# Optimization experiments

Hardware: AMD Instinct MI355X
Metric: run time of the kernel (lower is better)

## Reference

```python
import jax, jax.numpy as jnp
import numpy as np

NEG_INF = -jnp.inf
EPS = 1e-12  # F.normalize eps


def _build_spans(text_mask_row, max_span_length):
    # text_mask_row: concrete bool array [S]. Returns static numpy span index arrays.
    pos = np.nonzero(np.asarray(text_mask_row))[0]
    n = pos.size
    starts, ends, lens = [], [], []
    for i in range(n):
        for j in range(i, min(i + max_span_length, n)):
            starts.append(pos[i]); ends.append(pos[j]); lens.append(j - i + 1)
    return (np.asarray(starts, np.int32), np.asarray(ends, np.int32), np.asarray(lens, np.int32))


def setup_inputs() -> dict:
    key = jax.random.key(0)
    ks = jax.random.split(key, 8)
    B, S, H, T = 16, 1024, 768, 64
    L, LE = 4, 32
    Din = 3 * H + LE
    return {
        "hidden_states": jax.random.normal(ks[0], (B, S, H), jnp.float32),
        "topic_hidden": jax.random.normal(ks[1], (B, T, H), jnp.float32),
        "topic_mask": jnp.ones((B, T), jnp.bool_),
        "text_mask": jnp.ones((B, S), jnp.bool_),
        "len_emb": jax.random.normal(ks[2], (L + 1, LE), jnp.float32) * 0.02,
        "W1": jax.random.normal(ks[3], (Din, H), jnp.float32) / np.sqrt(Din),
        "b1": jnp.zeros((H,), jnp.float32),
        "W2": jax.random.normal(ks[4], (H, H), jnp.float32) / np.sqrt(H),
        "b2": jnp.zeros((H,), jnp.float32),
    }


def _l2norm(x):
    n = jnp.sqrt(jnp.sum(x * x, axis=-1, keepdims=True))
    return x / jnp.maximum(n, EPS)


def reference(hidden_states, topic_hidden, topic_mask, text_mask, len_emb, W1, b1, W2, b2):
    B, S, H = hidden_states.shape
    max_span_length = len_emb.shape[0] - 1
    # Masks are identical across the batch (all ones here): build spans once.
    starts_np, ends_np, lens_np = _build_spans(text_mask[0], max_span_length)
    starts = jnp.asarray(starts_np); ends = jnp.asarray(ends_np); lens = jnp.asarray(lens_np)
    N = starts.shape[0]

    start_v = hidden_states[:, starts]          # [B,N,H] gather span starts
    end_v = hidden_states[:, ends]              # [B,N,H] gather span ends
    csum = jnp.concatenate([jnp.zeros((B, 1, H), hidden_states.dtype),
                            jnp.cumsum(hidden_states, axis=1)], axis=1)  # [B,S+1,H]
    mean_v = (csum[:, ends + 1] - csum[:, starts]) / lens[None, :, None].astype(hidden_states.dtype)
    len_v = jnp.broadcast_to(len_emb[lens][None], (B, N, len_emb.shape[1]))

    feat = jnp.concatenate([start_v, end_v, mean_v, len_v], axis=-1)  # [B,N,3H+LE]
    span_vec = jax.nn.gelu(feat @ W1 + b1, approximate=False) @ W2 + b2  # [B,N,H]
    span_vec = _l2norm(span_vec)
    topic_vec = _l2norm(topic_hidden)                                    # [B,T,H]

    sim = jnp.einsum('bth,bnh->btn', topic_vec, span_vec)                # [B,T,N]
    sim = jnp.where(topic_mask[:, :, None], sim, NEG_INF)
    span_scores = jnp.max(sim, axis=1)                                   # [B,N]

    tok = jnp.arange(S)
    cover = (tok[None, :] >= starts[:, None]) & (tok[None, :] <= ends[:, None])  # [N,S]
    token_scores = jnp.max(jnp.where(cover[None], span_scores[:, :, None], NEG_INF), axis=1)  # [B,S]
    token_scores = jnp.where(text_mask, token_scores, NEG_INF)
    return token_scores
```

## Files before the change

### kernel.cpp

```cpp
#include <hip/hip_runtime.h>
#include <hip/hip_bf16.h>
#include <math.h>

typedef __bf16 bf16s;
typedef __attribute__((ext_vector_type(8))) __bf16 bf16x8;
typedef __attribute__((ext_vector_type(4))) __bf16 bf16x4;
typedef __attribute__((ext_vector_type(4))) float f32x4;

#define B_   16
#define S_   1024
#define H_   768
#define T_   64
#define L_   4
#define LE_  32
#define NPAD 4096
#define BS   (B_*S_)
#define BNR  (B_*NPAD)
#define N3   (3*H_)

static __device__ __forceinline__ void gload_lds16(const void* g, void* l) {
  __builtin_amdgcn_global_load_lds(
      (const __attribute__((address_space(1))) void*)g,
      (__attribute__((address_space(3))) void*)l, 16, 0, 0);
}

__global__ __launch_bounds__(1024) void k_build_spans(
    const int* __restrict__ text_mask,
    int* __restrict__ R, int* __restrict__ pos, int* __restrict__ spoff,
    int* __restrict__ starts, int* __restrict__ ends, int* __restrict__ lens,
    int* __restrict__ meta)
{
  __shared__ int buf[S_];
  int t = threadIdx.x;
  int m = text_mask[t] ? 1 : 0;
  buf[t] = m;
  __syncthreads();
  for (int off = 1; off < S_; off <<= 1) {
    int v = buf[t];
    if (t >= off) v += buf[t - off];
    __syncthreads();
    buf[t] = v;
    __syncthreads();
  }
  int incl = buf[t];
  R[t] = incl;
  if (m) pos[incl - 1] = t;
  int n = buf[S_ - 1];
  __syncthreads();
  int cnt = (t < n) ? min(L_, n - t) : 0;
  buf[t] = cnt;
  __syncthreads();
  for (int off = 1; off < S_; off <<= 1) {
    int v = buf[t];
    if (t >= off) v += buf[t - off];
    __syncthreads();
    buf[t] = v;
    __syncthreads();
  }
  int inc2 = buf[t];
  int base = inc2 - cnt;
  spoff[t] = base;
  if (t == 0) { meta[0] = buf[S_ - 1]; meta[1] = n; }
  __syncthreads();
  if (t < n) {
    int p0 = pos[t];
    for (int k = 0; k < cnt; k++) {
      starts[base + k] = p0;
      ends[base + k]   = pos[t + k];
      lens[base + k]   = k + 1;
    }
  }
}

__global__ __launch_bounds__(256) void k_prep(
    const float* __restrict__ hid, bf16s* __restrict__ hidb,
    const float* __restrict__ W1, bf16s* __restrict__ wbt,
    const float* __restrict__ W2, bf16s* __restrict__ w2t, bf16s* __restrict__ w2c,
    const float* __restrict__ lemb, float* __restrict__ LT,
    const float* __restrict__ TH, const float* __restrict__ b2,
    bf16s* __restrict__ TN, float* __restrict__ cvec)
{
  __shared__ float tile[64][65];
  __shared__ float red[256];
  int bid = blockIdx.x;
  int t = threadIdx.x;
  if (bid < 12288) {
    int i = bid * 256 + t;
    f32x4 v = ((const f32x4*)hid)[i];
    bf16x4 o;
    o[0] = (__bf16)v[0]; o[1] = (__bf16)v[1]; o[2] = (__bf16)v[2]; o[3] = (__bf16)v[3];
    ((bf16x4*)hidb)[i] = o;
  } else if (bid < 12864) {
    int local = bid - 12288;
    int c = local / 144, rem = local % 144;
    const float* in = (c < 3) ? (W1 + (size_t)c * H_ * H_) : W2;
    bf16s* out = (c < 3) ? (wbt + (size_t)c * H_ * H_) : w2t;
    int r0 = (rem / 12) * 64, c0 = (rem % 12) * 64;
    int tr = t >> 4, tc = (t & 15) * 4;
#pragma unroll
    for (int i = 0; i < 4; i++) {
      int row = tr + i * 16;
      f32x4 v = *(const f32x4*)(in + (long)(r0 + row) * H_ + c0 + tc);
      tile[row][tc+0] = v[0]; tile[row][tc+1] = v[1];
      tile[row][tc+2] = v[2]; tile[row][tc+3] = v[3];
    }
    __syncthreads();
#pragma unroll
    for (int i = 0; i < 4; i++) {
      int cc = tr + i * 16;
      bf16x4 o;
      o[0] = (__bf16)tile[tc+0][cc]; o[1] = (__bf16)tile[tc+1][cc];
      o[2] = (__bf16)tile[tc+2][cc]; o[3] = (__bf16)tile[tc+3][cc];
      *(bf16x4*)(out + (long)(c0 + cc) * H_ + r0 + tc) = o;
    }
  } else if (bid < 13440) {
    int i = (bid - 12864) * 256 + t;
    f32x4 v = ((const f32x4*)W2)[i];
    bf16x4 o;
    o[0] = (__bf16)v[0]; o[1] = (__bf16)v[1]; o[2] = (__bf16)v[2]; o[3] = (__bf16)v[3];
    ((bf16x4*)w2c)[i] = o;
  } else if (bid < 13455) {
    int idx = (bid - 13440) * 256 + t;
    if (idx < (L_ + 1) * H_) {
      int l = idx / H_, h = idx % H_;
      float acc = 0.f;
#pragma unroll
      for (int e = 0; e < LE_; e++) acc += lemb[l * LE_ + e] * W1[(long)(N3 + e) * H_ + h];
      LT[idx] = acc;
    }
  } else {
    int r = bid - 13455;
    const float* row = TH + (long)r * H_;
    float v0 = row[t], v1 = row[t + 256], v2 = row[t + 512];
    red[t] = v0 * v0 + v1 * v1 + v2 * v2;
    __syncthreads();
    for (int off = 128; off; off >>= 1) {
      if (t < off) red[t] += red[t + off];
      __syncthreads();
    }
    float rn = 1.0f / fmaxf(sqrtf(red[0]), 1e-12f);
    bf16s* o = TN + (long)r * H_;
    o[t] = (__bf16)(v0 * rn); o[t + 256] = (__bf16)(v1 * rn); o[t + 512] = (__bf16)(v2 * rn);
    __syncthreads();
    red[t] = v0 * b2[t] + v1 * b2[t + 256] + v2 * b2[t + 512];
    __syncthreads();
    for (int off = 128; off; off >>= 1) {
      if (t < off) red[t] += red[t + off];
      __syncthreads();
    }
    if (t == 0) cvec[r] = red[0] * rn;
  }
}

#define BKT 64
#define STG_A(kt_, h_) do { \
    const bf16s* s_ = gA + (long)(h_) * 128 * K + (long)(kt_) * BKT; \
    char* d_ = sA + ((kt_) & 1) * 32768 + (h_) * 16384 + wid * 1024; \
    gload_lds16(s_, d_); \
    gload_lds16(s_ + 64L * K, d_ + 8192); \
  } while (0)
#define STG_B(ct_, kt_, h_) do { \
    const bf16s* s_ = gB + (long)(ct_) * 256 * K + (long)(h_) * 128 * K + (long)(kt_) * BKT; \
    char* d_ = sB + ((kt_) & 1) * 32768 + (h_) * 16384 + wid * 1024; \
    gload_lds16(s_, d_); \
    gload_lds16(s_ + 64L * K, d_ + 8192); \
  } while (0)
#define MFMA_Q(AF_, FR0_, FC_) do { \
    _Pragma("unroll") \
    for (int f_ = 0; f_ < 4; ++f_) { \
      acc[FR0_+f_][FC_] = __builtin_amdgcn_mfma_f32_16x16x32_bf16(bfv[FC_][0], AF_[f_][0], acc[FR0_+f_][FC_], 0, 0, 0); \
      acc[FR0_+f_][FC_] = __builtin_amdgcn_mfma_f32_16x16x32_bf16(bfv[FC_][1], AF_[f_][1], acc[FR0_+f_][FC_], 0, 0, 0); \
    } } while (0)
#define PH_PRE()  __builtin_amdgcn_s_barrier(); \
                  asm volatile("s_waitcnt lgkmcnt(0)" ::: "memory"); \
                  __builtin_amdgcn_s_setprio(1)
#define PH_POST() __builtin_amdgcn_s_setprio(0); \
                  __builtin_amdgcn_s_barrier()

#define CHAIN_CORE(EPILOG_) \
  const char* aP0 = sA + wr * 16384; \
  const char* aP1 = aP0 + 32768; \
  const char* bP0 = sB + (wc >> 1) * 16384 + (wc & 1) * 8192; \
  const char* bP1 = bP0 + 32768; \
  int lrow = (l & 15) * 128; \
  int ls0 = (((l >> 4) ^ (l & 7)) * 16); \
  f32x4 acc[8][4]; \
  _Pragma("unroll") \
  for (int i_ = 0; i_ < 8; i_++) \
    _Pragma("unroll") \
    for (int j_ = 0; j_ < 4; j_++) acc[i_][j_] = (f32x4){0.f, 0.f, 0.f, 0.f}; \
  STG_B(0, 0, 0); STG_B(0, 0, 1); STG_A(0, 0); STG_A(0, 1); \
  STG_B(0, 1, 0); STG_B(0, 1, 1); STG_A(1, 0); \
  asm volatile("s_waitcnt vmcnt(6)" ::: "memory"); \
  __builtin_amdgcn_s_barrier(); \
  for (int s = 0; s < 3; ++s) { \
    for (int it = 0; it < 6; ++it) { \
      int kt0 = 2 * it; \
      bool nl = !(s == 2 && it == 5); \
      int ctn = (it == 5) ? s + 1 : s; \
      int kn0 = (it == 5) ? 0 : kt0 + 2; \
      int kn1 = (it == 5) ? 1 : kt0 + 3; \
      bf16x8 af0[4][2], af1[4][2], bfv[4][2]; \
       \
      _Pragma("unroll") \
      for (int f = 0; f < 4; ++f) { \
        af0[f][0] = *(const bf16x8*)(aP0 + f * 2048 + lrow + ls0); \
        af0[f][1] = *(const bf16x8*)(aP0 + f * 2048 + lrow + (ls0 ^ 64)); \
      } \
      _Pragma("unroll") \
      for (int c = 0; c < 4; ++c) { \
        bfv[c][0] = *(const bf16x8*)(bP0 + c * 2048 + lrow + ls0); \
        bfv[c][1] = *(const bf16x8*)(bP0 + c * 2048 + lrow + (ls0 ^ 64)); \
      } \
      STG_A(kt0 + 1, 1); \
      PH_PRE(); \
      MFMA_Q(af0, 0, 0); MFMA_Q(af0, 0, 1); \
      PH_POST(); \
       \
      if (nl) STG_B(ctn, kn0, 0); \
      PH_PRE(); \
      MFMA_Q(af0, 0, 2); MFMA_Q(af0, 0, 3); \
      PH_POST(); \
       \
      _Pragma("unroll") \
      for (int f = 0; f < 4; ++f) { \
        af1[f][0] = *(const bf16x8*)(aP0 + (f + 4) * 2048 + lrow + ls0); \
        af1[f][1] = *(const bf16x8*)(aP0 + (f + 4) * 2048 + lrow + (ls0 ^ 64)); \
      } \
      if (nl) STG_B(ctn, kn0, 1); \
      PH_PRE(); \
      MFMA_Q(af1, 4, 0); MFMA_Q(af1, 4, 1); \
      PH_POST(); \
       \
      if (nl) { STG_A(kn0, 0); asm volatile("s_waitcnt vmcnt(6)" ::: "memory"); } \
      else    { asm volatile("s_waitcnt vmcnt(0)" ::: "memory"); } \
      PH_PRE(); \
      MFMA_Q(af1, 4, 2); MFMA_Q(af1, 4, 3); \
      PH_POST(); \
       \
      _Pragma("unroll") \
      for (int f = 0; f < 4; ++f) { \
        af0[f][0] = *(const bf16x8*)(aP1 + f * 2048 + lrow + ls0); \
        af0[f][1] = *(const bf16x8*)(aP1 + f * 2048 + lrow + (ls0 ^ 64)); \
      } \
      _Pragma("unroll") \
      for (int c = 0; c < 4; ++c) { \
        bfv[c][0] = *(const bf16x8*)(bP1 + c * 2048 + lrow + ls0); \
        bfv[c][1] = *(const bf16x8*)(bP1 + c * 2048 + lrow + (ls0 ^ 64)); \
      } \
      if (nl) STG_A(kn0, 1); \
      PH_PRE(); \
      MFMA_Q(af0, 0, 0); MFMA_Q(af0, 0, 1); \
      PH_POST(); \
       \
      if (nl) STG_B(ctn, kn1, 0); \
      PH_PRE(); \
      MFMA_Q(af0, 0, 2); MFMA_Q(af0, 0, 3); \
      PH_POST(); \
       \
      _Pragma("unroll") \
      for (int f = 0; f < 4; ++f) { \
        af1[f][0] = *(const bf16x8*)(aP1 + (f + 4) * 2048 + lrow + ls0); \
        af1[f][1] = *(const bf16x8*)(aP1 + (f + 4) * 2048 + lrow + (ls0 ^ 64)); \
      } \
      if (nl) STG_B(ctn, kn1, 1); \
      PH_PRE(); \
      MFMA_Q(af1, 4, 0); MFMA_Q(af1, 4, 1); \
      PH_POST(); \
       \
      if (nl) { STG_A(kn1, 0); asm volatile("s_waitcnt vmcnt(6)" ::: "memory"); } \
      else    { asm volatile("s_waitcnt vmcnt(0)" ::: "memory"); } \
      PH_PRE(); \
      MFMA_Q(af1, 4, 2); MFMA_Q(af1, 4, 3); \
      PH_POST(); \
    } \
    EPILOG_(s); \
  }

__global__ __launch_bounds__(512, 1) void k_gemm1u(
    const bf16s* __restrict__ Ah, const bf16s* __restrict__ Bth, bf16s* __restrict__ Ch,
    const bf16s* __restrict__ Au, const bf16s* __restrict__ Btu, bf16s* __restrict__ Cu)
{
  __shared__ __align__(16) char sA[65536];
  __shared__ __align__(16) char sB[65536];
  __shared__ __align__(16) char sC[16384];
  const int K = H_;
  int bid = blockIdx.x;
  const bf16s *A, *Bt;
  bf16s* C;
  long a0, b0base;
  int NN;
  if (bid < 192) {
    int nid = (bid & 7) * 24 + (bid >> 3);
    A = Ah; Bt = Bth; C = Ch; NN = N3;
    a0 = (long)(nid / 3) * 256;
    b0base = (long)(nid % 3) * 768;
  } else {
    A = Au; Bt = Btu; C = Cu; NN = H_;
    a0 = (long)(bid - 192) * 256;
    b0base = 0;
  }
  int tid = threadIdx.x;
  int wid = tid >> 6, l = tid & 63;
  int wr = wid >> 2, wc = wid & 3;
  int srow = tid >> 3;
  int sslot = (tid & 7) ^ (srow & 7);
  const bf16s* gA = A + (a0 + srow) * (long)K + sslot * 8;
  const bf16s* gB = Bt + (b0base + srow) * (long)K + sslot * 8;

#define EPI_C(s_) do { \
    long cb = b0base + (s_) * 256; \
    _Pragma("unroll") \
    for (int e = 0; e < 8; ++e) { \
      if (wr == (e >> 2)) { \
        int f0 = (e & 3) * 2; \
        _Pragma("unroll") \
        for (int ff = 0; ff < 2; ++ff) { \
          int fr = f0 + ff; \
          int row_l = ff * 16 + (l & 15); \
          _Pragma("unroll") \
          for (int fc = 0; fc < 4; ++fc) { \
            int col2 = (wc * 64 + fc * 16 + (l >> 4) * 4) * 2; \
            bf16x4 o; \
            _Pragma("unroll") \
            for (int r = 0; r < 4; ++r) o[r] = (__bf16)acc[fr][fc][r]; \
            *(bf16x4*)(sC + ((row_l * 512 + col2) ^ ((row_l & 7) << 4))) = o; \
          } \
        } \
      } \
      __syncthreads(); \
      _Pragma("unroll") \
      for (int pp = 0; pp < 2; ++pp) { \
        int off = pp * 8192 + tid * 16; \
        int row_l = off >> 9; \
        bf16x8 v = *(const bf16x8*)(sC + (off ^ ((row_l & 7) << 4))); \
        *(bf16x8*)(C + (a0 + e * 32 + row_l) * (long)NN + cb + ((off & 511) >> 1)) = v; \
      } \
      __syncthreads(); \
    } \
    _Pragma("unroll") \
    for (int i_ = 0; i_ < 8; i_++) \
      _Pragma("unroll") \
      for (int j_ = 0; j_ < 4; j_++) acc[i_][j_] = (f32x4){0.f, 0.f, 0.f, 0.f}; \
  } while (0)

  CHAIN_CORE(EPI_C)
#undef EPI_C
}

__global__ __launch_bounds__(512, 1) void k_gemmnorm(
    const bf16s* __restrict__ Ax, const bf16s* __restrict__ Btw,
    const float* __restrict__ bias, float* __restrict__ ssbuf)
{
  __shared__ __align__(16) char sA[65536];
  __shared__ __align__(16) char sB[65536];
  const int K = H_;
  int bid = blockIdx.x;
  int nid = (bid & 7) * 32 + (bid >> 3);
  long a0 = (long)nid * 256;
  long b0base = 0;
  int tid = threadIdx.x;
  int wid = tid >> 6, l = tid & 63;
  int wr = wid >> 2, wc = wid & 3;
  int srow = tid >> 3;
  int sslot = (tid & 7) ^ (srow & 7);
  const bf16s* gA = Ax + (a0 + srow) * (long)K + sslot * 8;
  const bf16s* gB = Btw + (b0base + srow) * (long)K + sslot * 8;
  float ssp[8] = {0.f, 0.f, 0.f, 0.f, 0.f, 0.f, 0.f, 0.f};

#define EPI_N(s_) do { \
    f32x4 bb[4]; \
    _Pragma("unroll") \
    for (int fc = 0; fc < 4; ++fc) \
      bb[fc] = *(const f32x4*)(bias + (s_) * 256 + wc * 64 + fc * 16 + (l >> 4) * 4); \
    _Pragma("unroll") \
    for (int fr = 0; fr < 8; ++fr) { \
      float p = 0.f; \
      _Pragma("unroll") \
      for (int fc = 0; fc < 4; ++fc) { \
        _Pragma("unroll") \
        for (int r = 0; r < 4; ++r) { \
          float y = acc[fr][fc][r] + bb[fc][r]; \
          p += y * y; \
        } \
        acc[fr][fc] = (f32x4){0.f, 0.f, 0.f, 0.f}; \
      } \
      ssp[fr] += p; \
    } \
  } while (0)

  CHAIN_CORE(EPI_N)
#undef EPI_N

  float* sred = (float*)sA;
#pragma unroll
  for (int fr = 0; fr < 8; ++fr) {
    float p = ssp[fr];
    p += __shfl_xor(p, 16);
    p += __shfl_xor(p, 32);
    if (l < 16) sred[wc * 256 + wr * 128 + fr * 16 + l] = p;
  }
  __syncthreads();
  if (tid < 256) {
    ssbuf[a0 + tid] = sred[tid] + sred[256 + tid] + sred[512 + tid] + sred[768 + tid];
  }
}

#undef CHAIN_CORE
#undef STG_A
#undef STG_B
#undef MFMA_Q
#undef PH_PRE
#undef PH_POST

__global__ __launch_bounds__(256) void k_z1(
    const bf16s* __restrict__ P,
    const float* __restrict__ LT, const float* __restrict__ b1,
    const int* __restrict__ starts, const int* __restrict__ ends,
    const int* __restrict__ lens, const int* __restrict__ meta,
    bf16s* __restrict__ X)
{
  int idx = blockIdx.x * 256 + threadIdx.x;
  int h8 = idx % 96; int rest = idx / 96;
  int nid = rest % NPAD; int b = rest / NPAD;
  int h = h8 * 8;
  int N = meta[0];
  long orow = (long)(b * NPAD + nid) * H_ + h;
  if (nid >= N) {
    bf16x8 z;
#pragma unroll
    for (int j = 0; j < 8; j++) z[j] = (__bf16)0.f;
    *(bf16x8*)(X + orow) = z;
    return;
  }
  int sa = starts[nid], se = ends[nid], ln = lens[nid];
  float il = 1.0f / (float)ln;
  bf16x8 vs = *(const bf16x8*)(P + (long)(b * S_ + sa) * N3 + h);
  bf16x8 ve = *(const bf16x8*)(P + (long)(b * S_ + se) * N3 + H_ + h);
  float mv[8] = {0.f, 0.f, 0.f, 0.f, 0.f, 0.f, 0.f, 0.f};
  for (int i = sa; i <= se; i++) {
    bf16x8 vc = *(const bf16x8*)(P + (long)(b * S_ + i) * N3 + 2 * H_ + h);
#pragma unroll
    for (int j = 0; j < 8; j++) mv[j] += (float)vc[j];
  }
  f32x4 lt0 = *(const f32x4*)(LT + (long)ln * H_ + h);
  f32x4 lt1 = *(const f32x4*)(LT + (long)ln * H_ + h + 4);
  f32x4 bb0 = *(const f32x4*)(b1 + h);
  f32x4 bb1 = *(const f32x4*)(b1 + h + 4);
  bf16x8 o;
#pragma unroll
  for (int j = 0; j < 8; j++) {
    float ltv = (j < 4) ? lt0[j] : lt1[j - 4];
    float bbv = (j < 4) ? bb0[j] : bb1[j - 4];
    float x = (float)vs[j] + (float)ve[j] + mv[j] * il + ltv + bbv;
    float g = 0.5f * x * (1.0f + erff(x * 0.70710678118654752f));
    o[j] = (__bf16)g;
  }
  *(bf16x8*)(X + orow) = o;
}

__global__ __launch_bounds__(256) void k_simx(
    const bf16s* __restrict__ X, const bf16s* __restrict__ U,
    const float* __restrict__ cvec, const float* __restrict__ ssbuf,
    const int* __restrict__ tmask, float* __restrict__ scores)
{
  int b = blockIdx.y;
  int wid = threadIdx.x >> 6, l = threadIdx.x & 63;
  int st = blockIdx.x * 4 + wid;
  int span = st * 16 + (l & 15);
  const bf16s* xrow = X + (long)(b * NPAD + span) * H_ + (l >> 4) * 8;
  const bf16s* ubase = U + (long)b * T_ * H_ + (l >> 4) * 8;
  f32x4 acc[4];
#pragma unroll
  for (int tt = 0; tt < 4; tt++) acc[tt] = (f32x4){0.f, 0.f, 0.f, 0.f};
  for (int kk = 0; kk < H_ / 32; kk++) {
    bf16x8 av = *(const bf16x8*)(xrow + kk * 32);
#pragma unroll
    for (int tt = 0; tt < 4; tt++) {
      bf16x8 bv = *(const bf16x8*)(ubase + (long)(tt * 16 + (l & 15)) * H_ + kk * 32);
      acc[tt] = __builtin_amdgcn_mfma_f32_16x16x32_bf16(av, bv, acc[tt], 0, 0, 0);
    }
  }
  const int* tm = tmask + b * T_;
  bool msk[4];
  float cv[4];
#pragma unroll
  for (int tt = 0; tt < 4; tt++) {
    int tcol = tt * 16 + (l & 15);
    msk[tt] = tm[tcol] != 0;
    cv[tt] = cvec[b * T_ + tcol];
  }
  float best[4];
#pragma unroll
  for (int r = 0; r < 4; r++) {
    float v = -INFINITY;
#pragma unroll
    for (int tt = 0; tt < 4; tt++) if (msk[tt]) v = fmaxf(v, acc[tt][r] + cv[tt]);
    best[r] = v;
  }
#pragma unroll
  for (int off = 8; off; off >>= 1)
#pragma unroll
    for (int r = 0; r < 4; r++) best[r] = fmaxf(best[r], __shfl_xor(best[r], off));
  if ((l & 15) == 0) {
    int srow = st * 16 + (l >> 4) * 4;
#pragma unroll
    for (int r = 0; r < 4; r++) {
      float ss = ssbuf[b * NPAD + srow + r];
      scores[b * NPAD + srow + r] = best[r] / fmaxf(sqrtf(ss), 1e-12f);
    }
  }
}

__global__ __launch_bounds__(256) void k_token(
    const int* __restrict__ text_mask,
    const int* __restrict__ R, const int* __restrict__ spoff,
    const int* __restrict__ meta, const float* __restrict__ scores,
    float* __restrict__ out)
{
  int idx = blockIdx.x * 256 + threadIdx.x;
  int s = idx % S_, b = idx / S_;
  if (!text_mask[b * S_ + s]) { out[idx] = -INFINITY; return; }
  int n = meta[1];
  int r1 = R[s];
  int le = r1 - 1;
  int ge = text_mask[s] ? (r1 - 1) : r1;
  float best = -INFINITY;
  if (le >= 0 && ge < n) {
    int i0 = max(0, ge - (L_ - 1));
    for (int i = i0; i <= le; i++) {
      int jmax = min(i + L_ - 1, n - 1);
      int off = spoff[i];
      for (int j = max(i, ge); j <= jmax; j++)
        best = fmaxf(best, scores[b * NPAD + off + (j - i)]);
    }
  }
  out[idx] = best;
}

__global__ __launch_bounds__(256) void k_sentinel(float* __restrict__ out) {
  int i = blockIdx.x * 256 + threadIdx.x;
  if (i < BS) out[i] = 12345.0f;
}

extern "C" void kernel_launch(void* const* d_in, const int* in_sizes, int n_in,
                              void* d_out, int out_size, void* d_ws, size_t ws_size,
                              hipStream_t stream) {
  const float* hid = (const float*)d_in[0];
  const float* th  = (const float*)d_in[1];
  const int* tmask = (const int*)d_in[2];
  const int* xmask = (const int*)d_in[3];
  const float* lemb = (const float*)d_in[4];
  const float* W1   = (const float*)d_in[5];
  const float* b1   = (const float*)d_in[6];
  const float* W2   = (const float*)d_in[7];
  const float* b2   = (const float*)d_in[8];
  float* out = (float*)d_out;

  char* w = (char*)d_ws;
  auto alloc = [&](size_t bytes) {
    char* p = w; w += (bytes + 255) & ~(size_t)255; return p;
  };
  bf16s* wbt   = (bf16s*)alloc((size_t)N3 * H_ * 2);
  bf16s* w2t   = (bf16s*)alloc((size_t)H_ * H_ * 2);
  bf16s* w2c   = (bf16s*)alloc((size_t)H_ * H_ * 2);
  float* LT    = (float*)alloc((size_t)(L_ + 1) * H_ * 4);
  bf16s* topn  = (bf16s*)alloc((size_t)B_ * T_ * H_ * 2);
  bf16s* U     = (bf16s*)alloc((size_t)B_ * T_ * H_ * 2);
  float* cvec  = (float*)alloc((size_t)B_ * T_ * 4);
  float* ssbuf = (float*)alloc((size_t)BNR * 4);
  float* scores= (float*)alloc((size_t)B_ * NPAD * 4);
  int* R       = (int*)alloc(S_ * 4);
  int* pos     = (int*)alloc(S_ * 4);
  int* spoff   = (int*)alloc(S_ * 4);
  int* starts  = (int*)alloc(NPAD * 4);
  int* ends    = (int*)alloc(NPAD * 4);
  int* lens    = (int*)alloc(NPAD * 4);
  int* meta    = (int*)alloc(2 * 4);
  char* regionA = alloc((size_t)BS * H_ * 2 + (size_t)BS * N3 * 2);
  bf16s* hidb  = (bf16s*)regionA;
  bf16s* P     = (bf16s*)(regionA + (size_t)BS * H_ * 2);
  bf16s* X     = (bf16s*)alloc((size_t)BNR * H_ * 2);

  size_t required = (size_t)(w - (char*)d_ws);
  if (required > ws_size) {
    k_sentinel<<<(BS + 255) / 256, 256, 0, stream>>>(out);
    return;
  }

  k_build_spans<<<1, 1024, 0, stream>>>(xmask, R, pos, spoff, starts, ends, lens, meta);
  k_prep<<<14479, 256, 0, stream>>>(hid, hidb, W1, wbt, W2, w2t, w2c,
                                    lemb, LT, th, b2, topn, cvec);

  k_gemm1u<<<196, 512, 0, stream>>>(hidb, wbt, P, topn, w2c, U);

  k_z1<<<(BNR * 96) / 256, 256, 0, stream>>>(P, LT, b1, starts, ends, lens, meta, X);

  k_gemmnorm<<<256, 512, 0, stream>>>(X, w2t, b2, ssbuf);

  k_simx<<<dim3(NPAD / 64, B_), 256, 0, stream>>>(X, U, cvec, ssbuf, tmask, scores);
  k_token<<<(B_ * S_) / 256, 256, 0, stream>>>(xmask, R, spoff, meta, scores, out);
  (void)in_sizes; (void)n_in; (void)out_size;
}
```

Baseline: 322.1 us.

## Split first GEMM into per-tile blocks and fuse span-feature build per start token

```diff
diff --git a/kernel.cpp b/kernel.cpp
--- a/kernel.cpp
+++ b/kernel.cpp
@@ -153,14 +153,14 @@
 }
 
 #define BKT 64
-#define STG_A(kt_, h_) do { \
+#define STG1_A(kt_, h_) do { \
     const bf16s* s_ = gA + (long)(h_) * 128 * K + (long)(kt_) * BKT; \
     char* d_ = sA + ((kt_) & 1) * 32768 + (h_) * 16384 + wid * 1024; \
     gload_lds16(s_, d_); \
     gload_lds16(s_ + 64L * K, d_ + 8192); \
   } while (0)
-#define STG_B(ct_, kt_, h_) do { \
-    const bf16s* s_ = gB + (long)(ct_) * 256 * K + (long)(h_) * 128 * K + (long)(kt_) * BKT; \
+#define STG1_B(kt_, h_) do { \
+    const bf16s* s_ = gB + (long)(h_) * 128 * K + (long)(kt_) * BKT; \
     char* d_ = sB + ((kt_) & 1) * 32768 + (h_) * 16384 + wid * 1024; \
     gload_lds16(s_, d_); \
     gload_lds16(s_ + 64L * K, d_ + 8192); \
@@ -176,6 +176,176 @@
                   __builtin_amdgcn_s_setprio(1)
 #define PH_POST() __builtin_amdgcn_s_setprio(0); \
                   __builtin_amdgcn_s_barrier()
+
+__global__ __launch_bounds__(512, 2) void k_gemm8p(
+    const bf16s* __restrict__ Ah, const bf16s* __restrict__ Bth, bf16s* __restrict__ Ch,
+    const bf16s* __restrict__ Au, const bf16s* __restrict__ Btu, bf16s* __restrict__ Cu)
+{
+  __shared__ __align__(16) char sA[65536];
+  __shared__ __align__(16) char sB[65536];
+  const int K = H_;
+
+  int nwg = gridDim.x, bid = blockIdx.x;
+  int q = nwg >> 3, rr = nwg & 7;
+  int xcd = bid & 7, ix = bid >> 3;
+  int nid = (xcd < rr ? xcd * (q + 1) : rr * (q + 1) + (xcd - rr) * q) + ix;
+
+  const bf16s *A, *Bt;
+  bf16s* C;
+  long a0, b0;
+  int NN;
+  if (nid < 576) {
+    A = Ah; Bt = Bth; C = Ch; NN = N3;
+    a0 = (long)(nid / 9) * 256;
+    b0 = (long)(nid % 9) * 256;
+  } else {
+    int u = nid - 576;
+    A = Au; Bt = Btu; C = Cu; NN = H_;
+    a0 = (long)(u / 3) * 256;
+    b0 = (long)(u % 3) * 256;
+  }
+
+  int tid = threadIdx.x;
+  int wid = tid >> 6, l = tid & 63;
+  int wr = wid >> 2, wc = wid & 3;
+
+  int srow = tid >> 3;
+  int sslot = (tid & 7) ^ (srow & 7);
+  const bf16s* gA = A + (a0 + srow) * (long)K + sslot * 8;
+  const bf16s* gB = Bt + (b0 + srow) * (long)K + sslot * 8;
+
+  const char* aP0 = sA + wr * 16384;
+  const char* aP1 = aP0 + 32768;
+  const char* bP0 = sB + (wc >> 1) * 16384 + (wc & 1) * 8192;
+  const char* bP1 = bP0 + 32768;
+  int lrow = (l & 15) * 128;
+  int ls0 = (((l >> 4) ^ (l & 7)) * 16);
+
+  f32x4 acc[8][4];
+#pragma unroll
+  for (int i = 0; i < 8; i++)
+#pragma unroll
+    for (int j = 0; j < 4; j++) acc[i][j] = (f32x4){0.f, 0.f, 0.f, 0.f};
+
+  int NT = K / BKT;
+  int NITER = NT / 2;
+
+  STG1_B(0, 0); STG1_B(0, 1); STG1_A(0, 0); STG1_A(0, 1);
+  STG1_B(1, 0); STG1_B(1, 1); STG1_A(1, 0);
+  asm volatile("s_waitcnt vmcnt(6)" ::: "memory");
+  __builtin_amdgcn_s_barrier();
+
+  for (int it = 0; it < NITER; ++it) {
+    int t0 = 2 * it, t1 = t0 + 1;
+    bool nl = (it != NITER - 1);
+    bf16x8 af0[4][2], af1[4][2], bfv[4][2];
+
+#pragma unroll
+    for (int f = 0; f < 4; ++f) {
+      af0[f][0] = *(const bf16x8*)(aP0 + f * 2048 + lrow + ls0);
+      af0[f][1] = *(const bf16x8*)(aP0 + f * 2048 + lrow + (ls0 ^ 64));
+    }
+#pragma unroll
+    for (int c = 0; c < 4; ++c) {
+      bfv[c][0] = *(const bf16x8*)(bP0 + c * 2048 + lrow + ls0);
+      bfv[c][1] = *(const bf16x8*)(bP0 + c * 2048 + lrow + (ls0 ^ 64));
+    }
+    STG1_A(t1, 1);
+    PH_PRE();
+    MFMA_Q(af0, 0, 0); MFMA_Q(af0, 0, 1);
+    PH_POST();
+
+    if (nl) STG1_B(t0 + 2, 0);
+    PH_PRE();
+    MFMA_Q(af0, 0, 2); MFMA_Q(af0, 0, 3);
+    PH_POST();
+
+#pragma unroll
+    for (int f = 0; f < 4; ++f) {
+      af1[f][0] = *(const bf16x8*)(aP0 + (f + 4) * 2048 + lrow + ls0);
+      af1[f][1] = *(const bf16x8*)(aP0 + (f + 4) * 2048 + lrow + (ls0 ^ 64));
+    }
+    if (nl) STG1_B(t0 + 2, 1);
+    PH_PRE();
+    MFMA_Q(af1, 4, 0); MFMA_Q(af1, 4, 1);
+    PH_POST();
+
+    if (nl) { STG1_A(t0 + 2, 0); asm volatile("s_waitcnt vmcnt(6)" ::: "memory"); }
+    else    { asm volatile("s_waitcnt vmcnt(0)" ::: "memory"); }
+    PH_PRE();
+    MFMA_Q(af1, 4, 2); MFMA_Q(af1, 4, 3);
+    PH_POST();
+
+#pragma unroll
+    for (int f = 0; f < 4; ++f) {
+      af0[f][0] = *(const bf16x8*)(aP1 + f * 2048 + lrow + ls0);
+      af0[f][1] = *(const bf16x8*)(aP1 + f * 2048 + lrow + (ls0 ^ 64));
+    }
+#pragma unroll
+    for (int c = 0; c < 4; ++c) {
+      bfv[c][0] = *(const bf16x8*)(bP1 + c * 2048 + lrow + ls0);
+      bfv[c][1] = *(const bf16x8*)(bP1 + c * 2048 + lrow + (ls0 ^ 64));
+    }
+    if (nl) STG1_A(t0 + 2, 1);
+    PH_PRE();
+    MFMA_Q(af0, 0, 0); MFMA_Q(af0, 0, 1);
+    PH_POST();
+
+    if (nl) STG1_B(t1 + 2, 0);
+    PH_PRE();
+    MFMA_Q(af0, 0, 2); MFMA_Q(af0, 0, 3);
+    PH_POST();
+
+#pragma unroll
+    for (int f = 0; f < 4; ++f) {
+      af1[f][0] = *(const bf16x8*)(aP1 + (f + 4) * 2048 + lrow + ls0);
+      af1[f][1] = *(const bf16x8*)(aP1 + (f + 4) * 2048 + lrow + (ls0 ^ 64));
+    }
+    if (nl) STG1_B(t1 + 2, 1);
+    PH_PRE();
+    MFMA_Q(af1, 4, 0); MFMA_Q(af1, 4, 1);
+    PH_POST();
+
+    if (nl) { STG1_A(t1 + 2, 0); asm volatile("s_waitcnt vmcnt(6)" ::: "memory"); }
+    else    { asm volatile("s_waitcnt vmcnt(0)" ::: "memory"); }
+    PH_PRE();
+    MFMA_Q(af1, 4, 2); MFMA_Q(af1, 4, 3);
+    PH_POST();
+  }
+
+#pragma unroll
+  for (int fc = 0; fc < 4; fc++) {
+    long n0 = b0 + wc * 64 + fc * 16 + (l >> 4) * 4;
+#pragma unroll
+    for (int fr = 0; fr < 8; fr++) {
+      long mrow = a0 + wr * 128 + fr * 16 + (l & 15);
+      bf16x4 o;
+#pragma unroll
+      for (int r = 0; r < 4; r++) o[r] = (__bf16)acc[fr][fc][r];
+      *(bf16x4*)(C + mrow * (long)NN + n0) = o;
+    }
+  }
+}
+
+#define STG_A(kt_, h_) do { \
+    const bf16s* s_ = gA + (long)(h_) * 128 * K + (long)(kt_) * BKT; \
+    char* d_ = sA + ((kt_) & 1) * 32768 + (h_) * 16384 + wid * 1024; \
+    gload_lds16(s_, d_); \
+    gload_lds16(s_ + 64L * K, d_ + 8192); \
+  } while (0)
+#define STG_B(ct_, kt_, h_) do { \
+    const bf16s* s_ = gB + (long)(ct_) * 256 * K + (long)(h_) * 128 * K + (long)(kt_) * BKT; \
+    char* d_ = sB + ((kt_) & 1) * 32768 + (h_) * 16384 + wid * 1024; \
+    gload_lds16(s_, d_); \
+    gload_lds16(s_ + 8192); \
+  } while (0)
+#undef STG_B
+#define STG_B(ct_, kt_, h_) do { \
+    const bf16s* s_ = gB + (long)(ct_) * 256 * K + (long)(h_) * 128 * K + (long)(kt_) * BKT; \
+    char* d_ = sB + ((kt_) & 1) * 32768 + (h_) * 16384 + wid * 1024; \
+    gload_lds16(s_, d_); \
+    gload_lds16(s_ + 64L * K, d_ + 8192); \
+  } while (0)
 
 #define CHAIN_CORE(EPILOG_) \
   const char* aP0 = sA + wr * 16384; \
@@ -201,7 +371,6 @@
       int kn0 = (it == 5) ? 0 : kt0 + 2; \
       int kn1 = (it == 5) ? 1 : kt0 + 3; \
       bf16x8 af0[4][2], af1[4][2], bfv[4][2]; \
-       \
       _Pragma("unroll") \
       for (int f = 0; f < 4; ++f) { \
         af0[f][0] = *(const bf16x8*)(aP0 + f * 2048 + lrow + ls0); \
@@ -216,12 +385,10 @@
       PH_PRE(); \
       MFMA_Q(af0, 0, 0); MFMA_Q(af0, 0, 1); \
       PH_POST(); \
-       \
       if (nl) STG_B(ctn, kn0, 0); \
       PH_PRE(); \
       MFMA_Q(af0, 0, 2); MFMA_Q(af0, 0, 3); \
       PH_POST(); \
-       \
       _Pragma("unroll") \
       for (int f = 0; f < 4; ++f) { \
         af1[f][0] = *(const bf16x8*)(aP0 + (f + 4) * 2048 + lrow + ls0); \
@@ -231,13 +398,11 @@
       PH_PRE(); \
       MFMA_Q(af1, 4, 0); MFMA_Q(af1, 4, 1); \
       PH_POST(); \
-       \
       if (nl) { STG_A(kn0, 0); asm volatile("s_waitcnt vmcnt(6)" ::: "memory"); } \
       else    { asm volatile("s_waitcnt vmcnt(0)" ::: "memory"); } \
       PH_PRE(); \
       MFMA_Q(af1, 4, 2); MFMA_Q(af1, 4, 3); \
       PH_POST(); \
-       \
       _Pragma("unroll") \
       for (int f = 0; f < 4; ++f) { \
         af0[f][0] = *(const bf16x8*)(aP1 + f * 2048 + lrow + ls0); \
@@ -252,12 +417,10 @@
       PH_PRE(); \
       MFMA_Q(af0, 0, 0); MFMA_Q(af0, 0, 1); \
       PH_POST(); \
-       \
       if (nl) STG_B(ctn, kn1, 0); \
       PH_PRE(); \
       MFMA_Q(af0, 0, 2); MFMA_Q(af0, 0, 3); \
       PH_POST(); \
-       \
       _Pragma("unroll") \
       for (int f = 0; f < 4; ++f) { \
         af1[f][0] = *(const bf16x8*)(aP1 + (f + 4) * 2048 + lrow + ls0); \
@@ -267,7 +430,6 @@
       PH_PRE(); \
       MFMA_Q(af1, 4, 0); MFMA_Q(af1, 4, 1); \
       PH_POST(); \
-       \
       if (nl) { STG_A(kn1, 0); asm volatile("s_waitcnt vmcnt(6)" ::: "memory"); } \
       else    { asm volatile("s_waitcnt vmcnt(0)" ::: "memory"); } \
       PH_PRE(); \
@@ -276,77 +438,6 @@
     } \
     EPILOG_(s); \
   }
-
-__global__ __launch_bounds__(512, 1) void k_gemm1u(
-    const bf16s* __restrict__ Ah, const bf16s* __restrict__ Bth, bf16s* __restrict__ Ch,
-    const bf16s* __restrict__ Au, const bf16s* __restrict__ Btu, bf16s* __restrict__ Cu)
-{
-  __shared__ __align__(16) char sA[65536];
-  __shared__ __align__(16) char sB[65536];
-  __shared__ __align__(16) char sC[16384];
-  const int K = H_;
-  int bid = blockIdx.x;
-  const bf16s *A, *Bt;
-  bf16s* C;
-  long a0, b0base;
-  int NN;
-  if (bid < 192) {
-    int nid = (bid & 7) * 24 + (bid >> 3);
-    A = Ah; Bt = Bth; C = Ch; NN = N3;
-    a0 = (long)(nid / 3) * 256;
-    b0base = (long)(nid % 3) * 768;
-  } else {
-    A = Au; Bt = Btu; C = Cu; NN = H_;
-    a0 = (long)(bid - 192) * 256;
-    b0base = 0;
-  }
-  int tid = threadIdx.x;
-  int wid = tid >> 6, l = tid & 63;
-  int wr = wid >> 2, wc = wid & 3;
-  int srow = tid >> 3;
-  int sslot = (tid & 7) ^ (srow & 7);
-  const bf16s* gA = A + (a0 + srow) * (long)K + sslot * 8;
-  const bf16s* gB = Bt + (b0base + srow) * (long)K + sslot * 8;
-
-#define EPI_C(s_) do { \
-    long cb = b0base + (s_) * 256; \
-    _Pragma("unroll") \
-    for (int e = 0; e < 8; ++e) { \
-      if (wr == (e >> 2)) { \
-        int f0 = (e & 3) * 2; \
-        _Pragma("unroll") \
-        for (int ff = 0; ff < 2; ++ff) { \
-          int fr = f0 + ff; \
-          int row_l = ff * 16 + (l & 15); \
-          _Pragma("unroll") \
-          for (int fc = 0; fc < 4; ++fc) { \
-            int col2 = (wc * 64 + fc * 16 + (l >> 4) * 4) * 2; \
-            bf16x4 o; \
-            _Pragma("unroll") \
-            for (int r = 0; r < 4; ++r) o[r] = (__bf16)acc[fr][fc][r]; \
-            *(bf16x4*)(sC + ((row_l * 512 + col2) ^ ((row_l & 7) << 4))) = o; \
-          } \
-        } \
-      } \
-      __syncthreads(); \
-      _Pragma("unroll") \
-      for (int pp = 0; pp < 2; ++pp) { \
-        int off = pp * 8192 + tid * 16; \
-        int row_l = off >> 9; \
-        bf16x8 v = *(const bf16x8*)(sC + (off ^ ((row_l & 7) << 4))); \
-        *(bf16x8*)(C + (a0 + e * 32 + row_l) * (long)NN + cb + ((off & 511) >> 1)) = v; \
-      } \
-      __syncthreads(); \
-    } \
-    _Pragma("unroll") \
-    for (int i_ = 0; i_ < 8; i_++) \
-      _Pragma("unroll") \
-      for (int j_ = 0; j_ < 4; j_++) acc[i_][j_] = (f32x4){0.f, 0.f, 0.f, 0.f}; \
-  } while (0)
-
-  CHAIN_CORE(EPI_C)
-#undef EPI_C
-}
 
 __global__ __launch_bounds__(512, 1) void k_gemmnorm(
     const bf16s* __restrict__ Ax, const bf16s* __restrict__ Btw,
@@ -409,54 +500,66 @@
 #undef CHAIN_CORE
 #undef STG_A
 #undef STG_B
+#undef STG1_A
+#undef STG1_B
 #undef MFMA_Q
 #undef PH_PRE
 #undef PH_POST
 
-__global__ __launch_bounds__(256) void k_z1(
+__global__ __launch_bounds__(192) void k_z1(
     const bf16s* __restrict__ P,
     const float* __restrict__ LT, const float* __restrict__ b1,
-    const int* __restrict__ starts, const int* __restrict__ ends,
-    const int* __restrict__ lens, const int* __restrict__ meta,
-    bf16s* __restrict__ X)
+    const int* __restrict__ pos, const int* __restrict__ spoff,
+    const int* __restrict__ meta, bf16s* __restrict__ X)
 {
-  int idx = blockIdx.x * 256 + threadIdx.x;
-  int h8 = idx % 96; int rest = idx / 96;
-  int nid = rest % NPAD; int b = rest / NPAD;
-  int h = h8 * 8;
-  int N = meta[0];
-  long orow = (long)(b * NPAD + nid) * H_ + h;
-  if (nid >= N) {
-    bf16x8 z;
-#pragma unroll
-    for (int j = 0; j < 8; j++) z[j] = (__bf16)0.f;
-    *(bf16x8*)(X + orow) = z;
-    return;
-  }
-  int sa = starts[nid], se = ends[nid], ln = lens[nid];
-  float il = 1.0f / (float)ln;
-  bf16x8 vs = *(const bf16x8*)(P + (long)(b * S_ + sa) * N3 + h);
-  bf16x8 ve = *(const bf16x8*)(P + (long)(b * S_ + se) * N3 + H_ + h);
-  float mv[8] = {0.f, 0.f, 0.f, 0.f, 0.f, 0.f, 0.f, 0.f};
-  for (int i = sa; i <= se; i++) {
-    bf16x8 vc = *(const bf16x8*)(P + (long)(b * S_ + i) * N3 + 2 * H_ + h);
-#pragma unroll
-    for (int j = 0; j < 8; j++) mv[j] += (float)vc[j];
-  }
-  f32x4 lt0 = *(const f32x4*)(LT + (long)ln * H_ + h);
-  f32x4 lt1 = *(const f32x4*)(LT + (long)ln * H_ + h + 4);
-  f32x4 bb0 = *(const f32x4*)(b1 + h);
-  f32x4 bb1 = *(const f32x4*)(b1 + h + 4);
-  bf16x8 o;
-#pragma unroll
-  for (int j = 0; j < 8; j++) {
-    float ltv = (j < 4) ? lt0[j] : lt1[j - 4];
-    float bbv = (j < 4) ? bb0[j] : bb1[j - 4];
-    float x = (float)vs[j] + (float)ve[j] + mv[j] * il + ltv + bbv;
-    float g = 0.5f * x * (1.0f + erff(x * 0.70710678118654752f));
-    o[j] = (__bf16)g;
-  }
-  *(bf16x8*)(X + orow) = o;
+  int bid = blockIdx.x;
+  int t = threadIdx.x;
+  int h = t * 4;
+  if (bid < BS) {
+    int b = bid >> 10, i = bid & (S_ - 1);
+    int n = meta[1];
+    if (i >= n) return;
+    int cnt = min(L_, n - i);
+    int sa = pos[i];
+    int base = spoff[i];
+    const bf16s* Pb = P + (long)b * S_ * N3;
+    bf16x4 vs = *(const bf16x4*)(Pb + (long)sa * N3 + h);
+    f32x4 bb = *(const f32x4*)(b1 + h);
+    float run[4] = {0.f, 0.f, 0.f, 0.f};
+    int r = sa;
+    for (int k = 0; k < cnt; ++k) {
+      int se = pos[i + k];
+      for (; r <= se; ++r) {
+        bf16x4 vm = *(const bf16x4*)(Pb + (long)r * N3 + 2 * H_ + h);
+#pragma unroll
+        for (int j = 0; j < 4; j++) run[j] += (float)vm[j];
+      }
+      bf16x4 ve = *(const bf16x4*)(Pb + (long)se * N3 + H_ + h);
+      f32x4 lt = *(const f32x4*)(LT + (long)(k + 1) * H_ + h);
+      float il = 1.0f / (float)(k + 1);
+      bf16x4 o;
+#pragma unroll
+      for (int j = 0; j < 4; j++) {
+        float x = (float)vs[j] + (float)ve[j] + run[j] * il + lt[j] + bb[j];
+        float g = 0.5f * x * (1.0f + erff(x * 0.70710678118654752f));
+        o[j] = (__bf16)g;
+      }
+      *(bf16x4*)(X + ((long)b * NPAD + base + k) * H_ + h) = o;
+    }
+  } else {
+    int N = meta[0];
+    int pad = NPAD - N;
+    if (pad <= 0) return;
+    long total = (long)B_ * pad * 192;
+    for (long idx = (long)(bid - BS) * 192 + t; idx < total; idx += 512L * 192) {
+      int h4 = (int)(idx % 192);
+      long rrw = idx / 192;
+      int pr = (int)(rrw % pad);
+      int bb2 = (int)(rrw / pad);
+      bf16x4 z; z[0] = z[1] = z[2] = z[3] = (__bf16)0.f;
+      *(bf16x4*)(X + ((long)bb2 * NPAD + N + pr) * H_ + h4 * 4) = z;
+    }
+  }
 }
 
 __global__ __launch_bounds__(256) void k_simx(
@@ -592,9 +695,9 @@
   k_prep<<<14479, 256, 0, stream>>>(hid, hidb, W1, wbt, W2, w2t, w2c,
                                     lemb, LT, th, b2, topn, cvec);
 
-  k_gemm1u<<<196, 512, 0, stream>>>(hidb, wbt, P, topn, w2c, U);
-
-  k_z1<<<(BNR * 96) / 256, 256, 0, stream>>>(P, LT, b1, starts, ends, lens, meta, X);
+  k_gemm8p<<<588, 512, 0, stream>>>(hidb, wbt, P, topn, w2c, U);
+
+  k_z1<<<BS + 512, 192, 0, stream>>>(P, LT, b1, pos, spoff, meta, X);
 
   k_gemmnorm<<<256, 512, 0, stream>>>(X, w2t, b2, ssbuf);
 
```

Result: faster. 302.5 us (-6.1%).
